# Optimization experiments

Measured on AMD Instinct MI355X. Metric: run time of the kernel, lower is better.

## Reference

```python
import jax, jax.numpy as jnp
import numpy as np

N_FEAT = 7          # input_vector_size
M = 3               # memberships per feature (hardcoded 3 in torch module)
FUZZ = M ** N_FEAT  # 2187, cartesian product size
MID = 512
NUM_CLASS = 10
BATCH = 4096

# Precompute cartesian-product index table: itertools.product over rows of u[i]
# (last feature index varies fastest). IDX[k, i] = which of the 3 memberships of
# feature i appears in combination k.
_k = np.arange(FUZZ)
IDX = ((_k[:, None] // (M ** np.arange(N_FEAT - 1, -1, -1))[None, :]) % M).astype(np.int32)  # [FUZZ, N_FEAT]


def setup_inputs() -> dict:
    key = jax.random.key(0)
    ks = jax.random.split(key, 8)
    x = jax.random.normal(ks[0], (BATCH, N_FEAT), dtype=jnp.float32)
    # Parameters (xavier-ish init for weights, ones for b/bais as in torch init)
    c = jax.random.uniform(ks[1], (N_FEAT, M), minval=-1.0, maxval=1.0, dtype=jnp.float32)
    b = jnp.ones((N_FEAT, M), dtype=jnp.float32)
    wei = jax.random.uniform(ks[2], (FUZZ * N_FEAT, FUZZ), minval=-0.01, maxval=0.01, dtype=jnp.float32)
    bais = jnp.ones((1,), dtype=jnp.float32)
    W1 = jax.random.normal(ks[3], (MID, FUZZ), dtype=jnp.float32) * (1.0 / np.sqrt(FUZZ))
    b1 = jnp.zeros((MID,), dtype=jnp.float32)
    W2 = jax.random.normal(ks[4], (FUZZ, MID), dtype=jnp.float32) * (1.0 / np.sqrt(MID))
    b2 = jnp.zeros((FUZZ,), dtype=jnp.float32)
    W3 = jax.random.normal(ks[5], (NUM_CLASS, FUZZ), dtype=jnp.float32) * (1.0 / np.sqrt(FUZZ))
    b3 = jnp.zeros((NUM_CLASS,), dtype=jnp.float32)
    return {"x": x, "c": c, "b": b, "wei": wei, "bais": bais,
            "W1": W1, "b1": b1, "W2": W2, "b2": b2, "W3": W3, "b3": b3}


def reference(x, c, b, wei, bais, W1, b1, W2, b2, W3, b3):
    B = x.shape[0]
    # Gaussian fuzzy memberships: u[b, i, j] = exp(-(x[b,i]-c[i,j])^2 / b[i,j]^2)
    u = jnp.exp(-((x[:, :, None] - c[None]) ** 2) / (b[None] ** 2))  # [B, N_FEAT, M]
    # Cartesian product: dd[bt, k, i] = u[bt, i, IDX[k, i]]  (replaces itertools.product)
    idx = jnp.asarray(IDX)                       # [FUZZ, N_FEAT]
    feat = jnp.arange(N_FEAT)[None, :]           # [1, N_FEAT] broadcasts to [FUZZ, N_FEAT]
    dd = u[:, feat, idx]                         # [B, FUZZ, N_FEAT]
    # Fuzzy rule layer
    a = dd.reshape(B, FUZZ * N_FEAT) @ wei + bais            # [B, FUZZ]
    a_mean = a / jnp.sum(a, axis=1, keepdims=True)
    # Small residual MLP
    h1 = a_mean @ W1.T + b1                                   # [B, MID]
    h2 = h1 @ W2.T + b2                                       # [B, FUZZ]
    h3 = (a_mean + h2) @ W3.T + b3                            # [B, NUM_CLASS]
    out = jax.nn.leaky_relu(h3, negative_slope=0.2)
    # Dropout(0.5) omitted (eval mode / deterministic baseline)
    return out
```

## Files before the change

kernel.cpp:

```cpp
#include <hip/hip_runtime.h>

#define FUZZ 2187
#define NFEAT 7
#define MID 512
#define NCLS 10
#define BATCH 4096
#define SSTR 2192
#define NCHUNK 81
#define PROWS 13

__global__ __launch_bounds__(256) void k_reduce_wei(const float* __restrict__ wei,
                                                    float* __restrict__ Spart) {
    int n = blockIdx.x * 256 + threadIdx.x;
    if (n >= FUZZ) return;
    int by = blockIdx.y;

    float sum4[4];
    float acc9[9];
#pragma unroll
    for (int j = 0; j < 4; ++j) sum4[j] = 0.f;
#pragma unroll
    for (int r = 0; r < 9; ++r) acc9[r] = 0.f;

    const float* base = wei + (size_t)(by * 27) * 7 * FUZZ + n;
#pragma unroll
    for (int kk = 0; kk < 27; ++kk) {
        const float* rp = base + (size_t)kk * 7 * FUZZ;
        float v0 = rp[0];
        float v1 = rp[(size_t)1 * FUZZ];
        float v2 = rp[(size_t)2 * FUZZ];
        float v3 = rp[(size_t)3 * FUZZ];
        float v4 = rp[(size_t)4 * FUZZ];
        float v5 = rp[(size_t)5 * FUZZ];
        float v6 = rp[(size_t)6 * FUZZ];
        sum4[0] += v0;
        sum4[1] += v1;
        sum4[2] += v2;
        sum4[3] += v3;
        acc9[0 + (kk / 9)]       += v4;
        acc9[3 + ((kk / 3) % 3)] += v5;
        acc9[6 + (kk % 3)]       += v6;
    }

    float* outp = Spart + (size_t)by * PROWS * FUZZ + n;
#pragma unroll
    for (int j = 0; j < 4; ++j) outp[(size_t)j * FUZZ] = sum4[j];
#pragma unroll
    for (int r = 0; r < 9; ++r) outp[(size_t)(4 + r) * FUZZ] = acc9[r];
}

__global__ __launch_bounds__(256) void k_reduce2(const float* __restrict__ Spart,
                                                 float* __restrict__ S) {
    int n = blockIdx.x * 256 + threadIdx.x;
    if (n >= FUZZ) return;
    int t = blockIdx.y;
    float s;
    if (t < 12) {
        int j = t / 3, m = t % 3;
        const int places[4] = {27, 9, 3, 1};
        int ops[3];
        int o = 0;
#pragma unroll
        for (int q = 0; q < 4; ++q)
            if (q != j) ops[o++] = places[q];
        int byb = m * places[j];
        float s0 = 0.f, s1 = 0.f, s2 = 0.f;
#pragma unroll 9
        for (int c = 0; c < 27; c += 3) {
            int by0 = byb + (c / 9) * ops[0] + (((c + 0) / 3) % 3) * ops[1] + ((c + 0) % 3) * ops[2];
            int by1 = byb + (c / 9) * ops[0] + (((c + 1) / 3) % 3) * ops[1] + ((c + 1) % 3) * ops[2];
            int by2 = byb + (c / 9) * ops[0] + (((c + 2) / 3) % 3) * ops[1] + ((c + 2) % 3) * ops[2];
            s0 += Spart[((size_t)by0 * PROWS + j) * FUZZ + n];
            s1 += Spart[((size_t)by1 * PROWS + j) * FUZZ + n];
            s2 += Spart[((size_t)by2 * PROWS + j) * FUZZ + n];
        }
        s = s0 + s1 + s2;
    } else {
        int row = t - 8;
        float s0 = 0.f, s1 = 0.f, s2 = 0.f;
        for (int by = 0; by < 81; by += 3) {
            s0 += Spart[((size_t)(by + 0) * PROWS + row) * FUZZ + n];
            s1 += Spart[((size_t)(by + 1) * PROWS + row) * FUZZ + n];
            s2 += Spart[((size_t)(by + 2) * PROWS + row) * FUZZ + n];
        }
        s = s0 + s1 + s2;
    }
    S[t * SSTR + n] = s;
}

__device__ __forceinline__ float wave_sum(float v) {
#pragma unroll
    for (int off = 32; off > 0; off >>= 1) v += __shfl_down(v, off, 64);
    return v;
}

__global__ __launch_bounds__(256) void k_sw1(const float* __restrict__ S,
                                             const float* __restrict__ W1,
                                             float* __restrict__ SW1,
                                             float* __restrict__ ws1) {
    int i = blockIdx.x;
    int tid = threadIdx.x;
    float acc[21];
    float aw = 0.f;
#pragma unroll
    for (int t = 0; t < 21; ++t) acc[t] = 0.f;
    for (int n = tid; n < FUZZ; n += 256) {
        float w1 = W1[(size_t)i * FUZZ + n];
        aw += w1;
#pragma unroll
        for (int t = 0; t < 21; ++t) acc[t] += S[t * SSTR + n] * w1;
    }
#pragma unroll
    for (int t = 0; t < 21; ++t) acc[t] = wave_sum(acc[t]);
    aw = wave_sum(aw);
    __shared__ float red[4][22];
    int w = tid >> 6, lane = tid & 63;
    if (lane == 0) {
#pragma unroll
        for (int t = 0; t < 21; ++t) red[w][t] = acc[t];
        red[w][21] = aw;
    }
    __syncthreads();
    if (tid < 22) {
        float v = red[0][tid] + red[1][tid] + red[2][tid] + red[3][tid];
        if (tid < 21) SW1[tid * MID + i] = v;
        else          ws1[i] = v;
    }
}

__global__ __launch_bounds__(64) void k_g(const float* __restrict__ SW1,
                                          const float* __restrict__ ws1,
                                          const float* __restrict__ b1,
                                          const float* __restrict__ W2,
                                          float* __restrict__ G,
                                          float* __restrict__ q,
                                          float* __restrict__ p) {
    int n = blockIdx.x;
    int lane = threadIdx.x;
    float acc[21];
    float aq = 0.f, ap = 0.f;
#pragma unroll
    for (int t = 0; t < 21; ++t) acc[t] = 0.f;
    for (int i = lane; i < MID; i += 64) {
        float w2 = W2[(size_t)n * MID + i];
        aq += ws1[i] * w2;
        ap += b1[i] * w2;
#pragma unroll
        for (int t = 0; t < 21; ++t) acc[t] += SW1[t * MID + i] * w2;
    }
#pragma unroll
    for (int t = 0; t < 21; ++t) acc[t] = wave_sum(acc[t]);
    aq = wave_sum(aq);
    ap = wave_sum(ap);
    if (lane == 0) {
#pragma unroll
        for (int t = 0; t < 21; ++t) G[t * SSTR + n] = acc[t];
        q[n] = aq;
        p[n] = ap;
    }
}

__global__ __launch_bounds__(512) void k_h(const float* __restrict__ S,
                                           const float* __restrict__ G,
                                           const float* __restrict__ q,
                                           const float* __restrict__ p,
                                           const float* __restrict__ b2,
                                           const float* __restrict__ b3,
                                           const float* __restrict__ W3,
                                           float* __restrict__ H,
                                           float* __restrict__ v,
                                           float* __restrict__ w,
                                           float* __restrict__ T) {
    int c = blockIdx.x;
    int tid = threadIdx.x;
    int wv = tid >> 6, lane = tid & 63;
    __shared__ float red[8][24];
    float acc[21];
#pragma unroll
    for (int t = 0; t < 21; ++t) acc[t] = 0.f;
    if (c < NCLS) {
        float av = 0.f, aw = 0.f;
        for (int n = tid; n < FUZZ; n += 512) {
            float w3 = W3[(size_t)c * FUZZ + n];
            av += (1.0f + q[n]) * w3;
            aw += (p[n] + b2[n]) * w3;
#pragma unroll
            for (int t = 0; t < 21; ++t)
                acc[t] += (S[t * SSTR + n] + G[t * SSTR + n]) * w3;
        }
#pragma unroll
        for (int t = 0; t < 21; ++t) acc[t] = wave_sum(acc[t]);
        av = wave_sum(av);
        aw = wave_sum(aw);
        if (lane == 0) {
#pragma unroll
            for (int t = 0; t < 21; ++t) red[wv][t] = acc[t];
            red[wv][21] = av;
            red[wv][22] = aw;
        }
        __syncthreads();
        if (tid < 23) {
            float s = 0.f;
#pragma unroll
            for (int k = 0; k < 8; ++k) s += red[k][tid];
            if (tid < 21)      H[tid * NCLS + c] = s;
            else if (tid == 21) v[c] = s;
            else               w[c] = s + b3[c];
        }
    } else {
        for (int n = tid; n < FUZZ; n += 512) {
#pragma unroll
            for (int t = 0; t < 21; ++t) acc[t] += S[t * SSTR + n];
        }
#pragma unroll
        for (int t = 0; t < 21; ++t) acc[t] = wave_sum(acc[t]);
        if (lane == 0) {
#pragma unroll
            for (int t = 0; t < 21; ++t) red[wv][t] = acc[t];
        }
        __syncthreads();
        if (tid < 21) {
            float s = 0.f;
#pragma unroll
            for (int k = 0; k < 8; ++k) s += red[k][tid];
            T[tid] = s;
        }
    }
}

__global__ __launch_bounds__(256) void k_out(const float* __restrict__ x,
                                             const float* __restrict__ cc,
                                             const float* __restrict__ bbv,
                                             const float* __restrict__ bais,
                                             const float* __restrict__ T,
                                             const float* __restrict__ H,
                                             const float* __restrict__ v,
                                             const float* __restrict__ w,
                                             float* __restrict__ out) {
    int b = blockIdx.x * 256 + threadIdx.x;
    if (b >= BATCH) return;
    float xv[NFEAT];
#pragma unroll
    for (int j = 0; j < NFEAT; ++j) xv[j] = x[b * NFEAT + j];
    float u[21];
#pragma unroll
    for (int j = 0; j < NFEAT; ++j) {
#pragma unroll
        for (int m = 0; m < 3; ++m) {
            float d = xv[j] - cc[j * 3 + m];
            float bv = bbv[j * 3 + m];
            u[j * 3 + m] = expf(-(d * d) / (bv * bv));
        }
    }
    float ba = bais[0];
    float r = 2187.0f * ba;
#pragma unroll
    for (int t = 0; t < 21; ++t) r += u[t] * T[t];
    float inv = 1.0f / r;
#pragma unroll
    for (int c = 0; c < NCLS; ++c) {
        float s = 0.f;
#pragma unroll
        for (int t = 0; t < 21; ++t) s += u[t] * H[t * NCLS + c];
        float h = (s + ba * v[c]) * inv + w[c];
        out[b * NCLS + c] = (h >= 0.f) ? h : 0.2f * h;
    }
}

extern "C" void kernel_launch(void* const* d_in, const int* in_sizes, int n_in,
                              void* d_out, int out_size, void* d_ws, size_t ws_size,
                              hipStream_t stream) {
    const float* x    = (const float*)d_in[0];
    const float* c    = (const float*)d_in[1];
    const float* bbv  = (const float*)d_in[2];
    const float* wei  = (const float*)d_in[3];
    const float* bais = (const float*)d_in[4];
    const float* W1   = (const float*)d_in[5];
    const float* b1   = (const float*)d_in[6];
    const float* W2   = (const float*)d_in[7];
    const float* b2   = (const float*)d_in[8];
    const float* W3   = (const float*)d_in[9];
    const float* b3   = (const float*)d_in[10];

    float* ws    = (float*)d_ws;
    float* Spart = ws;
    float* S     = Spart + 2302912;
    float* G     = S + 21 * SSTR;
    float* SW1   = G + 21 * SSTR;
    float* ws1   = SW1 + 21 * MID;
    float* q     = ws1 + MID;
    float* p     = q + SSTR;
    float* T     = p + SSTR;
    float* H     = T + 32;
    float* v     = H + 224;
    float* w     = v + 16;

    k_reduce_wei<<<dim3(9, NCHUNK), 256, 0, stream>>>(wei, Spart);
    k_reduce2<<<dim3(9, 21), 256, 0, stream>>>(Spart, S);
    k_sw1<<<MID, 256, 0, stream>>>(S, W1, SW1, ws1);
    k_g<<<FUZZ, 64, 0, stream>>>(SW1, ws1, b1, W2, G, q, p);
    k_h<<<NCLS + 1, 512, 0, stream>>>(S, G, q, p, b2, b3, W3, H, v, w, T);
    k_out<<<(BATCH + 255) / 256, 256, 0, stream>>>(x, c, bbv, bais, T, H, v, w,
                                                   (float*)d_out);
}
```

Before: 310.0 us.

## Vectorize wei reduction with float4 loads and finer chunking, widen k_h blocks

```diff
diff --git a/kernel.cpp b/kernel.cpp
--- a/kernel.cpp
+++ b/kernel.cpp
@@ -6,86 +6,124 @@
 #define NCLS 10
 #define BATCH 4096
 #define SSTR 2192
-#define NCHUNK 81
-#define PROWS 13
-
-__global__ __launch_bounds__(256) void k_reduce_wei(const float* __restrict__ wei,
+#define NCH 243
+#define PROWS 11
+#define PSTR 2188
+#define NF4 546
+
+__device__ __forceinline__ void f4add(float4& a, const float4& b) {
+    a.x += b.x; a.y += b.y; a.z += b.z; a.w += b.w;
+}
+
+__global__ __launch_bounds__(192) void k_reduce_wei(const float* __restrict__ wei,
                                                     float* __restrict__ Spart) {
-    int n = blockIdx.x * 256 + threadIdx.x;
-    if (n >= FUZZ) return;
+    int n4 = blockIdx.x * 192 + threadIdx.x;
+    if (n4 > NF4) return;
     int by = blockIdx.y;
-
-    float sum4[4];
-    float acc9[9];
-#pragma unroll
-    for (int j = 0; j < 4; ++j) sum4[j] = 0.f;
-#pragma unroll
-    for (int r = 0; r < 9; ++r) acc9[r] = 0.f;
-
-    const float* base = wei + (size_t)(by * 27) * 7 * FUZZ + n;
-#pragma unroll
-    for (int kk = 0; kk < 27; ++kk) {
-        const float* rp = base + (size_t)kk * 7 * FUZZ;
-        float v0 = rp[0];
-        float v1 = rp[(size_t)1 * FUZZ];
-        float v2 = rp[(size_t)2 * FUZZ];
-        float v3 = rp[(size_t)3 * FUZZ];
-        float v4 = rp[(size_t)4 * FUZZ];
-        float v5 = rp[(size_t)5 * FUZZ];
-        float v6 = rp[(size_t)6 * FUZZ];
-        sum4[0] += v0;
-        sum4[1] += v1;
-        sum4[2] += v2;
-        sum4[3] += v3;
-        acc9[0 + (kk / 9)]       += v4;
-        acc9[3 + ((kk / 3) % 3)] += v5;
-        acc9[6 + (kk % 3)]       += v6;
-    }
-
-    float* outp = Spart + (size_t)by * PROWS * FUZZ + n;
-#pragma unroll
-    for (int j = 0; j < 4; ++j) outp[(size_t)j * FUZZ] = sum4[j];
-#pragma unroll
-    for (int r = 0; r < 9; ++r) outp[(size_t)(4 + r) * FUZZ] = acc9[r];
-}
-
-__global__ __launch_bounds__(256) void k_reduce2(const float* __restrict__ Spart,
+    const float* base = wei + (size_t)(by * 9) * 7 * FUZZ;
+    float* outp = Spart + (size_t)by * PROWS * PSTR;
+
+    if (n4 < NF4) {
+        float4 acc[PROWS];
+#pragma unroll
+        for (int r = 0; r < PROWS; ++r) acc[r] = make_float4(0.f, 0.f, 0.f, 0.f);
+#pragma unroll
+        for (int kk = 0; kk < 9; ++kk) {
+            const float* rp = base + (size_t)kk * 7 * FUZZ + 4 * n4;
+            float4 v0 = *(const float4*)(rp);
+            float4 v1 = *(const float4*)(rp + (size_t)1 * FUZZ);
+            float4 v2 = *(const float4*)(rp + (size_t)2 * FUZZ);
+            float4 v3 = *(const float4*)(rp + (size_t)3 * FUZZ);
+            float4 v4 = *(const float4*)(rp + (size_t)4 * FUZZ);
+            float4 v5 = *(const float4*)(rp + (size_t)5 * FUZZ);
+            float4 v6 = *(const float4*)(rp + (size_t)6 * FUZZ);
+            f4add(acc[0], v0);
+            f4add(acc[1], v1);
+            f4add(acc[2], v2);
+            f4add(acc[3], v3);
+            f4add(acc[4], v4);
+            f4add(acc[5 + kk / 3], v5);
+            f4add(acc[8 + kk % 3], v6);
+        }
+#pragma unroll
+        for (int r = 0; r < PROWS; ++r)
+            *(float4*)(outp + (size_t)r * PSTR + 4 * n4) = acc[r];
+    } else {
+        float acc[PROWS][3];
+#pragma unroll
+        for (int r = 0; r < PROWS; ++r)
+            for (int c = 0; c < 3; ++c) acc[r][c] = 0.f;
+#pragma unroll
+        for (int kk = 0; kk < 9; ++kk) {
+            const float* rp = base + (size_t)kk * 7 * FUZZ + 2184;
+#pragma unroll
+            for (int j = 0; j < 7; ++j) {
+                int row = (j < 5) ? j : ((j == 5) ? 5 + kk / 3 : 8 + kk % 3);
+#pragma unroll
+                for (int c = 0; c < 3; ++c)
+                    acc[row][c] += rp[(size_t)j * FUZZ + c];
+            }
+        }
+#pragma unroll
+        for (int r = 0; r < PROWS; ++r)
+            for (int c = 0; c < 3; ++c)
+                outp[(size_t)r * PSTR + 2184 + c] = acc[r][c];
+    }
+}
+
+__global__ __launch_bounds__(192) void k_reduce2(const float* __restrict__ Spart,
                                                  float* __restrict__ S) {
-    int n = blockIdx.x * 256 + threadIdx.x;
-    if (n >= FUZZ) return;
+    int n4 = blockIdx.x * 192 + threadIdx.x;
+    if (n4 > NF4) return;
     int t = blockIdx.y;
-    float s;
-    if (t < 12) {
-        int j = t / 3, m = t % 3;
-        const int places[4] = {27, 9, 3, 1};
-        int ops[3];
-        int o = 0;
-#pragma unroll
-        for (int q = 0; q < 4; ++q)
-            if (q != j) ops[o++] = places[q];
-        int byb = m * places[j];
+    int j = t / 3, m = t % 3;
+
+    if (n4 < NF4) {
+        float4 s = make_float4(0.f, 0.f, 0.f, 0.f);
+        if (j < 5) {
+            const int place[5] = {81, 27, 9, 3, 1};
+            int ops[4];
+            int o = 0;
+            for (int q = 0; q < 5; ++q)
+                if (q != j) ops[o++] = place[q];
+            int byb = m * place[j];
+            for (int c = 0; c < 81; ++c) {
+                int by = byb + (c / 27) * ops[0] + ((c / 9) % 3) * ops[1]
+                             + ((c / 3) % 3) * ops[2] + (c % 3) * ops[3];
+                f4add(s, *(const float4*)(Spart + ((size_t)by * PROWS + j) * PSTR + 4 * n4));
+            }
+        } else {
+            int row = (j == 5) ? 5 + m : 8 + m;
+            for (int by = 0; by < NCH; ++by)
+                f4add(s, *(const float4*)(Spart + ((size_t)by * PROWS + row) * PSTR + 4 * n4));
+        }
+        *(float4*)(S + (size_t)t * SSTR + 4 * n4) = s;
+    } else {
         float s0 = 0.f, s1 = 0.f, s2 = 0.f;
-#pragma unroll 9
-        for (int c = 0; c < 27; c += 3) {
-            int by0 = byb + (c / 9) * ops[0] + (((c + 0) / 3) % 3) * ops[1] + ((c + 0) % 3) * ops[2];
-            int by1 = byb + (c / 9) * ops[0] + (((c + 1) / 3) % 3) * ops[1] + ((c + 1) % 3) * ops[2];
-            int by2 = byb + (c / 9) * ops[0] + (((c + 2) / 3) % 3) * ops[1] + ((c + 2) % 3) * ops[2];
-            s0 += Spart[((size_t)by0 * PROWS + j) * FUZZ + n];
-            s1 += Spart[((size_t)by1 * PROWS + j) * FUZZ + n];
-            s2 += Spart[((size_t)by2 * PROWS + j) * FUZZ + n];
-        }
-        s = s0 + s1 + s2;
-    } else {
-        int row = t - 8;
-        float s0 = 0.f, s1 = 0.f, s2 = 0.f;
-        for (int by = 0; by < 81; by += 3) {
-            s0 += Spart[((size_t)(by + 0) * PROWS + row) * FUZZ + n];
-            s1 += Spart[((size_t)(by + 1) * PROWS + row) * FUZZ + n];
-            s2 += Spart[((size_t)(by + 2) * PROWS + row) * FUZZ + n];
-        }
-        s = s0 + s1 + s2;
-    }
-    S[t * SSTR + n] = s;
+        if (j < 5) {
+            const int place[5] = {81, 27, 9, 3, 1};
+            int ops[4];
+            int o = 0;
+            for (int q = 0; q < 5; ++q)
+                if (q != j) ops[o++] = place[q];
+            int byb = m * place[j];
+            for (int c = 0; c < 81; ++c) {
+                int by = byb + (c / 27) * ops[0] + ((c / 9) % 3) * ops[1]
+                             + ((c / 3) % 3) * ops[2] + (c % 3) * ops[3];
+                const float* p = Spart + ((size_t)by * PROWS + j) * PSTR + 2184;
+                s0 += p[0]; s1 += p[1]; s2 += p[2];
+            }
+        } else {
+            int row = (j == 5) ? 5 + m : 8 + m;
+            for (int by = 0; by < NCH; ++by) {
+                const float* p = Spart + ((size_t)by * PROWS + row) * PSTR + 2184;
+                s0 += p[0]; s1 += p[1]; s2 += p[2];
+            }
+        }
+        S[(size_t)t * SSTR + 2184] = s0;
+        S[(size_t)t * SSTR + 2185] = s1;
+        S[(size_t)t * SSTR + 2186] = s2;
+    }
 }
 
 __device__ __forceinline__ float wave_sum(float v) {
@@ -160,27 +198,27 @@
     }
 }
 
-__global__ __launch_bounds__(512) void k_h(const float* __restrict__ S,
-                                           const float* __restrict__ G,
-                                           const float* __restrict__ q,
-                                           const float* __restrict__ p,
-                                           const float* __restrict__ b2,
-                                           const float* __restrict__ b3,
-                                           const float* __restrict__ W3,
-                                           float* __restrict__ H,
-                                           float* __restrict__ v,
-                                           float* __restrict__ w,
-                                           float* __restrict__ T) {
+__global__ __launch_bounds__(1024) void k_h(const float* __restrict__ S,
+                                            const float* __restrict__ G,
+                                            const float* __restrict__ q,
+                                            const float* __restrict__ p,
+                                            const float* __restrict__ b2,
+                                            const float* __restrict__ b3,
+                                            const float* __restrict__ W3,
+                                            float* __restrict__ H,
+                                            float* __restrict__ v,
+                                            float* __restrict__ w,
+                                            float* __restrict__ T) {
     int c = blockIdx.x;
     int tid = threadIdx.x;
     int wv = tid >> 6, lane = tid & 63;
-    __shared__ float red[8][24];
+    __shared__ float red[16][24];
     float acc[21];
 #pragma unroll
     for (int t = 0; t < 21; ++t) acc[t] = 0.f;
     if (c < NCLS) {
         float av = 0.f, aw = 0.f;
-        for (int n = tid; n < FUZZ; n += 512) {
+        for (int n = tid; n < FUZZ; n += 1024) {
             float w3 = W3[(size_t)c * FUZZ + n];
             av += (1.0f + q[n]) * w3;
             aw += (p[n] + b2[n]) * w3;
@@ -202,13 +240,13 @@
         if (tid < 23) {
             float s = 0.f;
 #pragma unroll
-            for (int k = 0; k < 8; ++k) s += red[k][tid];
-            if (tid < 21)      H[tid * NCLS + c] = s;
+            for (int k = 0; k < 16; ++k) s += red[k][tid];
+            if (tid < 21)       H[tid * NCLS + c] = s;
             else if (tid == 21) v[c] = s;
-            else               w[c] = s + b3[c];
+            else                w[c] = s + b3[c];
         }
     } else {
-        for (int n = tid; n < FUZZ; n += 512) {
+        for (int n = tid; n < FUZZ; n += 1024) {
 #pragma unroll
             for (int t = 0; t < 21; ++t) acc[t] += S[t * SSTR + n];
         }
@@ -222,7 +260,7 @@
         if (tid < 21) {
             float s = 0.f;
 #pragma unroll
-            for (int k = 0; k < 8; ++k) s += red[k][tid];
+            for (int k = 0; k < 16; ++k) s += red[k][tid];
             T[tid] = s;
         }
     }
@@ -284,7 +322,7 @@
 
     float* ws    = (float*)d_ws;
     float* Spart = ws;
-    float* S     = Spart + 2302912;
+    float* S     = Spart + 5848528;
     float* G     = S + 21 * SSTR;
     float* SW1   = G + 21 * SSTR;
     float* ws1   = SW1 + 21 * MID;
@@ -295,11 +333,11 @@
     float* v     = H + 224;
     float* w     = v + 16;
 
-    k_reduce_wei<<<dim3(9, NCHUNK), 256, 0, stream>>>(wei, Spart);
-    k_reduce2<<<dim3(9, 21), 256, 0, stream>>>(Spart, S);
+    k_reduce_wei<<<dim3(3, NCH), 192, 0, stream>>>(wei, Spart);
+    k_reduce2<<<dim3(3, 21), 192, 0, stream>>>(Spart, S);
     k_sw1<<<MID, 256, 0, stream>>>(S, W1, SW1, ws1);
     k_g<<<FUZZ, 64, 0, stream>>>(SW1, ws1, b1, W2, G, q, p);
-    k_h<<<NCLS + 1, 512, 0, stream>>>(S, G, q, p, b2, b3, W3, H, v, w, T);
+    k_h<<<NCLS + 1, 1024, 0, stream>>>(S, G, q, p, b2, b3, W3, H, v, w, T);
     k_out<<<(BATCH + 255) / 256, 256, 0, stream>>>(x, c, bbv, bais, T, H, v, w,
                                                    (float*)d_out);
 }
```

Result: no change. 305.1 us (-1.6%).
